# Kernel optimization log

Hardware: AMD Instinct MI355X
Metric: run time of the kernel (lower is better)

The kernel has to match this reference:

```python
import jax, jax.numpy as jnp
import numpy as np

B, IN, H = 4096, 1024, 1024


def setup_inputs() -> dict:
    key = jax.random.key(0)
    ks = jax.random.split(key, 20)
    s_in = 1.0 / np.sqrt(IN)
    s_h = 1.0 / np.sqrt(H)
    def lin(kw, kb, fan_in, scale):
        W = jax.random.uniform(kw, (H, fan_in), jnp.float32, -scale, scale)
        b = jax.random.uniform(kb, (H,), jnp.float32, -scale, scale)
        return W, b
    Wxf, bxf = lin(ks[0], ks[1], IN, s_in)
    Whf, bhf = lin(ks[2], ks[3], H, s_h)
    Wxi, bxi = lin(ks[4], ks[5], IN, s_in)
    Whi, bhi = lin(ks[6], ks[7], H, s_h)
    Wxo, bxo = lin(ks[8], ks[9], IN, s_in)
    Who, bho = lin(ks[10], ks[11], H, s_h)
    Wxc, bxc = lin(ks[12], ks[13], IN, s_in)
    Whc, bhc = lin(ks[14], ks[15], H, s_h)
    x = jax.random.normal(ks[16], (B, IN), jnp.float32)
    c = jax.random.normal(ks[17], (B, H), jnp.float32)
    h = jax.random.normal(ks[18], (B, H), jnp.float32)
    return dict(x=x, c=c, h=h,
                Wxf=Wxf, bxf=bxf, Whf=Whf, bhf=bhf,
                Wxi=Wxi, bxi=bxi, Whi=Whi, bhi=bhi,
                Wxo=Wxo, bxo=bxo, Who=Who, bho=bho,
                Wxc=Wxc, bxc=bxc, Whc=Whc, bhc=bhc)


def reference(x, c, h,
              Wxf, bxf, Whf, bhf,
              Wxi, bxi, Whi, bhi,
              Wxo, bxo, Who, bho,
              Wxc, bxc, Whc, bhc):
    # Fuse the 8 small GEMMs into two batched GEMMs: x @ Wx^T and h @ Wh^T
    # with gate outputs concatenated along the hidden dim [f, i, o, c~].
    Wx = jnp.concatenate([Wxf, Wxi, Wxo, Wxc], axis=0)   # [4H, IN]
    Wh = jnp.concatenate([Whf, Whi, Who, Whc], axis=0)   # [4H, H]
    bx = jnp.concatenate([bxf, bxi, bxo, bxc], axis=0)   # [4H]
    bh = jnp.concatenate([bhf, bhi, bho, bhc], axis=0)   # [4H]
    gates = x @ Wx.T + h @ Wh.T + (bx + bh)              # [B, 4H]
    hs = Wxf.shape[0]
    f = jax.nn.sigmoid(gates[:, 0 * hs:1 * hs])
    i = jax.nn.sigmoid(gates[:, 1 * hs:2 * hs])
    o = jax.nn.sigmoid(gates[:, 2 * hs:3 * hs])
    ctil = jnp.tanh(gates[:, 3 * hs:4 * hs])
    ct = f * c + ctil * i
    ht = jnp.tanh(ct) * o
    return (ct, ht)
```

## Files before the change

kernel.cpp:

```cpp
#include <hip/hip_runtime.h>
#include <hip/hip_bf16.h>
#include <stdint.h>

typedef __hip_bfloat16 bf16;
typedef __attribute__((ext_vector_type(8))) short short8;
typedef __attribute__((ext_vector_type(16))) float floatx16;

#define AS1(p) ((const __attribute__((address_space(1))) void*)(p))
#define AS3(p) ((__attribute__((address_space(3))) void*)(p))

#define M_DIM 4096
#define H_DIM 1024
#define STAGE 24576

__device__ __forceinline__ unsigned short f2bf(float f) {
    uint32_t u = __float_as_uint(f);
    uint32_t r = (u + 0x7FFFu + ((u >> 16) & 1u)) >> 16;
    return (unsigned short)r;
}
__device__ __forceinline__ float fast_sigmoid(float v) {
    return 1.0f / (1.0f + __expf(-v));
}
__device__ __forceinline__ float fast_tanh(float v) {
    return 2.0f / (1.0f + __expf(-2.0f * v)) - 1.0f;
}

__global__ __launch_bounds__(256)
void pack_bf16(const float* __restrict__ x, const float* __restrict__ h,
               const float* Wxf, const float* Wxi, const float* Wxo, const float* Wxc,
               const float* Whf, const float* Whi, const float* Who, const float* Whc,
               unsigned short* __restrict__ ws)
{
    const int w = threadIdx.x >> 6;
    const int l = threadIdx.x & 63;
    const uint32_t W = blockIdx.x * 4u + (uint32_t)w;

    const uint32_t r  = (uint32_t)l & 31u;
    const uint32_t kh = (uint32_t)l >> 5;

    const float* src;
    uint32_t row, kq;
    if (W < 16384u) {
        const uint32_t ch4 = W & 3u;
        kq = (W >> 2) & 127u;
        const uint32_t mx = W >> 9;
        src = (kq < 64u) ? x : h;
        row = mx * 128u + ch4 * 32u + r;
    } else {
        const uint32_t V  = W - 16384u;
        kq = V & 127u;
        const uint32_t U  = V >> 7;
        const uint32_t b8 = U & 7u;
        const uint32_t ny = U >> 3;
        const uint32_t g  = b8 >> 1;
        const uint32_t nh = b8 & 1u;
        if (kq < 64u)
            src = (g == 0) ? Wxf : (g == 1) ? Wxi : (g == 2) ? Wxo : Wxc;
        else
            src = (g == 0) ? Whf : (g == 1) ? Whi : (g == 2) ? Who : Whc;
        row = ny * 64u + nh * 32u + r;
    }
    const float* s = src + (size_t)row * 1024u + (kq & 63u) * 16u + kh * 8u;
    const float4 v0 = *(const float4*)s;
    const float4 v1 = *(const float4*)(s + 4);
    short8 pk;
    pk[0] = (short)f2bf(v0.x); pk[1] = (short)f2bf(v0.y);
    pk[2] = (short)f2bf(v0.z); pk[3] = (short)f2bf(v0.w);
    pk[4] = (short)f2bf(v1.x); pk[5] = (short)f2bf(v1.y);
    pk[6] = (short)f2bf(v1.z); pk[7] = (short)f2bf(v1.w);
    *(short8*)(ws + (size_t)W * 512u + (uint32_t)l * 8u) = pk;
}

#define GLL(srcp, dstp) __builtin_amdgcn_global_load_lds(AS1(srcp), AS3(dstp), 16, 0, 0)
#define WAITB(N) do {                                                         \
    asm volatile("s_waitcnt vmcnt(" #N ") lgkmcnt(0)\ns_barrier" ::: "memory");\
    __builtin_amdgcn_sched_barrier(0);                                        \
} while (0)

#define MFMA32(a, b, c) __builtin_amdgcn_mfma_f32_32x32x16_bf16((a), (b), (c), 0, 0, 0)

#define ISSUE(SL) do {                                                        \
    GLL(p0, lds + (SL)*STAGE + loff0); p0 += ks0;                             \
    GLL(p1, lds + (SL)*STAGE + loff1); p1 += ks1;                             \
    GLL(p2, lds + (SL)*STAGE + loff2); p2 += ks2;                             \
} while (0)

#define COMPUTE(SC) do {                                                      \
    short8 a0_ = *(const short8*)(ldsA + (SC)*STAGE + 0);                     \
    short8 a1_ = *(const short8*)(ldsA + (SC)*STAGE + 1024);                  \
    short8 b0_ = *(const short8*)(ldsB + (SC)*STAGE + 0);                     \
    short8 b1_ = *(const short8*)(ldsB + (SC)*STAGE + 2048);                  \
    acc00 = MFMA32(a0_, b0_, acc00);                                          \
    acc01 = MFMA32(a1_, b0_, acc01);                                          \
    acc10 = MFMA32(a0_, b1_, acc10);                                          \
    acc11 = MFMA32(a1_, b1_, acc11);                                          \
    a0_ = *(const short8*)(ldsA + (SC)*STAGE + 4096);                         \
    a1_ = *(const short8*)(ldsA + (SC)*STAGE + 4096 + 1024);                  \
    b0_ = *(const short8*)(ldsB + (SC)*STAGE + 8192);                         \
    b1_ = *(const short8*)(ldsB + (SC)*STAGE + 8192 + 2048);                  \
    acc00 = MFMA32(a0_, b0_, acc00);                                          \
    acc01 = MFMA32(a1_, b0_, acc01);                                          \
    acc10 = MFMA32(a0_, b1_, acc10);                                          \
    acc11 = MFMA32(a1_, b1_, acc11);                                          \
} while (0)

#define ITER(SC, SL) do { WAITB(3); ISSUE(SL); COMPUTE(SC); } while (0)

__global__ __launch_bounds__(512, 4)
void lstm_fused_kernel(const unsigned short* __restrict__ ws,
                       const float* __restrict__ c,
                       const float* __restrict__ bxf, const float* __restrict__ bhf,
                       const float* __restrict__ bxi, const float* __restrict__ bhi,
                       const float* __restrict__ bxo, const float* __restrict__ bho,
                       const float* __restrict__ bxc, const float* __restrict__ bhc,
                       float* __restrict__ out)
{
    __shared__ __align__(16) char lds[3 * STAGE];

    const int tid  = threadIdx.x;
    const int w    = tid >> 6;
    const int lane = tid & 63;

    const int bid = blockIdx.x;
    const int mx  = bid >> 4;
    const int ny  = ((bid & 7) << 1) | ((bid >> 3) & 1);
    const int bm0 = mx * 128;
    const int bn0 = ny * 64;

    const int wM = w >> 2;
    const int wN = (w >> 1) & 1;
    const int gp = w & 1;

    const unsigned short* p0; const unsigned short* p1; const unsigned short* p2;
    uint32_t loff0, loff1, loff2, ks0, ks1, ks2;
#define CHDEC(CH, P, LO, KS) do {                                             \
    const int ch_ = (CH);                                                     \
    if (ch_ < 8) {                                                            \
        const uint32_t kc_ = (uint32_t)ch_ >> 2, c4_ = (uint32_t)ch_ & 3u;    \
        P = ws + ((uint32_t)mx * 512u + kc_ * 4u + c4_) * 512u                \
               + (uint32_t)lane * 8u;                                         \
        KS = 4096u;                                                           \
    } else {                                                                  \
        const uint32_t b_ = (uint32_t)(ch_ - 8), kc_ = b_ >> 3, b8_ = b_ & 7u;\
        P = ws + (16384u + ((uint32_t)ny * 8u + b8_) * 128u + kc_) * 512u     \
               + (uint32_t)lane * 8u;                                         \
        KS = 1024u;                                                           \
    }                                                                         \
    LO = (uint32_t)ch_ * 1024u;                                               \
} while (0)
    CHDEC(w * 3 + 0, p0, loff0, ks0);
    CHDEC(w * 3 + 1, p1, loff1, ks1);
    CHDEC(w * 3 + 2, p2, loff2, ks2);
#undef CHDEC

    const char* ldsA = lds + (uint32_t)lane * 16u + (uint32_t)wM * 2048u;
    const char* ldsB = lds + (uint32_t)lane * 16u + 8192u
                           + ((uint32_t)(4 * gp + wN)) * 1024u;

    floatx16 acc00 = {0}, acc01 = {0}, acc10 = {0}, acc11 = {0};

    ISSUE(0);
    ISSUE(1);

    for (int t = 0; t < 20; ++t) {
        ITER(0, 2); ITER(1, 0); ITER(2, 1);
    }
    ITER(0, 2);
    ITER(1, 0);
    WAITB(3); COMPUTE(2);
    WAITB(0); COMPUTE(0);

    const int colg = bn0 + (wN * 32) + (lane & 31);
    const int lq   = lane >> 5;
    const int wrow = wM * 64;
    float* out_ct = out;
    float* out_ht = out + (size_t)M_DIM * H_DIM;

    float bA, bB;
    if (gp == 0) { bA = bxf[colg] + bhf[colg]; bB = bxi[colg] + bhi[colg]; }
    else         { bA = bxo[colg] + bho[colg]; bB = bxc[colg] + bhc[colg]; }

    if (gp == 0) {
#pragma unroll
        for (int r = 0; r < 16; ++r) {
            acc00[r] = fast_sigmoid(acc00[r] + bA);
            acc01[r] = fast_sigmoid(acc01[r] + bA);
            acc10[r] = fast_sigmoid(acc10[r] + bB);
            acc11[r] = fast_sigmoid(acc11[r] + bB);
        }
    } else {
#pragma unroll
        for (int r = 0; r < 16; ++r) {
            acc00[r] = fast_sigmoid(acc00[r] + bA);
            acc01[r] = fast_sigmoid(acc01[r] + bA);
            acc10[r] = fast_tanh(acc10[r] + bB);
            acc11[r] = fast_tanh(acc11[r] + bB);
        }
    }

    __syncthreads();

    {
        char* wr = (char*)lds + (uint32_t)(w >> 1) * 16384u + (uint32_t)gp * 8192u;
        if (gp == 0) {
#pragma unroll
            for (int r = 0; r < 16; ++r) {
                const int ri = (r & 3) + 8 * (r >> 2) + 4 * lq;
                *(float*)(wr +        ri * 128 + (lane & 31) * 4) = acc01[r];
                *(float*)(wr + 4096 + ri * 128 + (lane & 31) * 4) = acc11[r];
            }
        } else {
#pragma unroll
            for (int r = 0; r < 16; ++r) {
                const int ri = (r & 3) + 8 * (r >> 2) + 4 * lq;
                *(float*)(wr +        ri * 128 + (lane & 31) * 4) = acc00[r];
                *(float*)(wr + 4096 + ri * 128 + (lane & 31) * 4) = acc10[r];
            }
        }
    }

    __syncthreads();

    {
        const char* rd = (const char*)lds + (uint32_t)(w >> 1) * 16384u
                                          + (uint32_t)(1 - gp) * 8192u;
        if (gp == 0) {
#pragma unroll
            for (int r = 0; r < 16; ++r) {
                const int ri = (r & 3) + 8 * (r >> 2) + 4 * lq;
                const float O  = *(const float*)(rd +        ri * 128 + (lane & 31) * 4);
                const float CT = *(const float*)(rd + 4096 + ri * 128 + (lane & 31) * 4);
                const int row = bm0 + wrow + ri;
                const float cv  = c[(size_t)row * H_DIM + colg];
                const float ctn = acc00[r] * cv + CT * acc10[r];
                const float htn = fast_tanh(ctn) * O;
                out_ct[(size_t)row * H_DIM + colg] = ctn;
                out_ht[(size_t)row * H_DIM + colg] = htn;
            }
        } else {
#pragma unroll
            for (int r = 0; r < 16; ++r) {
                const int ri = (r & 3) + 8 * (r >> 2) + 4 * lq;
                const float F = *(const float*)(rd +        ri * 128 + (lane & 31) * 4);
                const float I = *(const float*)(rd + 4096 + ri * 128 + (lane & 31) * 4);
                const int row = bm0 + wrow + 32 + ri;
                const float cv  = c[(size_t)row * H_DIM + colg];
                const float ctn = F * cv + acc11[r] * I;
                const float htn = fast_tanh(ctn) * acc01[r];
                out_ct[(size_t)row * H_DIM + colg] = ctn;
                out_ht[(size_t)row * H_DIM + colg] = htn;
            }
        }
    }
}

extern "C" void kernel_launch(void* const* d_in, const int* in_sizes, int n_in,
                              void* d_out, int out_size, void* d_ws, size_t ws_size,
                              hipStream_t stream) {
    (void)in_sizes; (void)n_in; (void)out_size; (void)ws_size;
    const float* x   = (const float*)d_in[0];
    const float* c   = (const float*)d_in[1];
    const float* h   = (const float*)d_in[2];
    const float* Wxf = (const float*)d_in[3];  const float* bxf = (const float*)d_in[4];
    const float* Whf = (const float*)d_in[5];  const float* bhf = (const float*)d_in[6];
    const float* Wxi = (const float*)d_in[7];  const float* bxi = (const float*)d_in[8];
    const float* Whi = (const float*)d_in[9];  const float* bhi = (const float*)d_in[10];
    const float* Wxo = (const float*)d_in[11]; const float* bxo = (const float*)d_in[12];
    const float* Who = (const float*)d_in[13]; const float* bho = (const float*)d_in[14];
    const float* Wxc = (const float*)d_in[15]; const float* bxc = (const float*)d_in[16];
    const float* Whc = (const float*)d_in[17]; const float* bhc = (const float*)d_in[18];
    float* out = (float*)d_out;
    unsigned short* ws = (unsigned short*)d_ws;

    pack_bf16<<<8192, 256, 0, stream>>>(x, h,
        Wxf, Wxi, Wxo, Wxc, Whf, Whi, Who, Whc, ws);

    lstm_fused_kernel<<<512, 512, 0, stream>>>(ws, c,
        bxf, bhf, bxi, bhi, bxo, bho, bxc, bhc, out);
}
```

Baseline: 247.5 us.

## Assign all four gates per wave to remove LDS epilogue exchange

Changes the per-wave MFMA tiling so each wave computes a 32x32 tile for all four gates (one A fragment, four B fragments) instead of a 64x64 tile for two gates. With f, i, o and c~ all held in the same wave's registers, the epilogue no longer needs two __syncthreads and an LDS round-trip to exchange gate values between paired waves. The cost is more LDS reads of B per MFMA in the main loop (one A read per four B reads instead of two A and two B), which changes LDS bandwidth pressure.

New measurement: 228.3 us. 1.08x faster.

```diff
diff --git a/kernel.cpp b/kernel.cpp
--- a/kernel.cpp
+++ b/kernel.cpp
@@ -86,22 +86,24 @@
 } while (0)
 
 #define COMPUTE(SC) do {                                                      \
-    short8 a0_ = *(const short8*)(ldsA + (SC)*STAGE + 0);                     \
-    short8 a1_ = *(const short8*)(ldsA + (SC)*STAGE + 1024);                  \
+    short8 a_  = *(const short8*)(ldsA + (SC)*STAGE + 0);                     \
     short8 b0_ = *(const short8*)(ldsB + (SC)*STAGE + 0);                     \
     short8 b1_ = *(const short8*)(ldsB + (SC)*STAGE + 2048);                  \
-    acc00 = MFMA32(a0_, b0_, acc00);                                          \
-    acc01 = MFMA32(a1_, b0_, acc01);                                          \
-    acc10 = MFMA32(a0_, b1_, acc10);                                          \
-    acc11 = MFMA32(a1_, b1_, acc11);                                          \
-    a0_ = *(const short8*)(ldsA + (SC)*STAGE + 4096);                         \
-    a1_ = *(const short8*)(ldsA + (SC)*STAGE + 4096 + 1024);                  \
+    short8 b2_ = *(const short8*)(ldsB + (SC)*STAGE + 4096);                  \
+    short8 b3_ = *(const short8*)(ldsB + (SC)*STAGE + 6144);                  \
+    acc0 = MFMA32(a_, b0_, acc0);                                             \
+    acc1 = MFMA32(a_, b1_, acc1);                                             \
+    acc2 = MFMA32(a_, b2_, acc2);                                             \
+    acc3 = MFMA32(a_, b3_, acc3);                                             \
+    a_  = *(const short8*)(ldsA + (SC)*STAGE + 4096);                         \
     b0_ = *(const short8*)(ldsB + (SC)*STAGE + 8192);                         \
     b1_ = *(const short8*)(ldsB + (SC)*STAGE + 8192 + 2048);                  \
-    acc00 = MFMA32(a0_, b0_, acc00);                                          \
-    acc01 = MFMA32(a1_, b0_, acc01);                                          \
-    acc10 = MFMA32(a0_, b1_, acc10);                                          \
-    acc11 = MFMA32(a1_, b1_, acc11);                                          \
+    b2_ = *(const short8*)(ldsB + (SC)*STAGE + 8192 + 4096);                  \
+    b3_ = *(const short8*)(ldsB + (SC)*STAGE + 8192 + 6144);                  \
+    acc0 = MFMA32(a_, b0_, acc0);                                             \
+    acc1 = MFMA32(a_, b1_, acc1);                                             \
+    acc2 = MFMA32(a_, b2_, acc2);                                             \
+    acc3 = MFMA32(a_, b3_, acc3);                                             \
 } while (0)
 
 #define ITER(SC, SL) do { WAITB(3); ISSUE(SL); COMPUTE(SC); } while (0)
@@ -127,9 +129,8 @@
     const int bm0 = mx * 128;
     const int bn0 = ny * 64;
 
-    const int wM = w >> 2;
-    const int wN = (w >> 1) & 1;
-    const int gp = w & 1;
+    const int wM2 = w >> 1;
+    const int wN  = w & 1;
 
     const unsigned short* p0; const unsigned short* p1; const unsigned short* p2;
     uint32_t loff0, loff1, loff2, ks0, ks1, ks2;
@@ -153,11 +154,10 @@
     CHDEC(w * 3 + 2, p2, loff2, ks2);
 #undef CHDEC
 
-    const char* ldsA = lds + (uint32_t)lane * 16u + (uint32_t)wM * 2048u;
-    const char* ldsB = lds + (uint32_t)lane * 16u + 8192u
-                           + ((uint32_t)(4 * gp + wN)) * 1024u;
-
-    floatx16 acc00 = {0}, acc01 = {0}, acc10 = {0}, acc11 = {0};
+    const char* ldsA = lds + (uint32_t)lane * 16u + (uint32_t)wM2 * 1024u;
+    const char* ldsB = lds + (uint32_t)lane * 16u + 8192u + (uint32_t)wN * 1024u;
+
+    floatx16 acc0 = {0}, acc1 = {0}, acc2 = {0}, acc3 = {0};
 
     ISSUE(0);
     ISSUE(1);
@@ -170,87 +170,30 @@
     WAITB(3); COMPUTE(2);
     WAITB(0); COMPUTE(0);
 
-    const int colg = bn0 + (wN * 32) + (lane & 31);
+    const int colg = bn0 + wN * 32 + (lane & 31);
     const int lq   = lane >> 5;
-    const int wrow = wM * 64;
+    const int row0 = bm0 + wM2 * 32;
     float* out_ct = out;
     float* out_ht = out + (size_t)M_DIM * H_DIM;
 
-    float bA, bB;
-    if (gp == 0) { bA = bxf[colg] + bhf[colg]; bB = bxi[colg] + bhi[colg]; }
-    else         { bA = bxo[colg] + bho[colg]; bB = bxc[colg] + bhc[colg]; }
-
-    if (gp == 0) {
+    const float bf_ = bxf[colg] + bhf[colg];
+    const float bi_ = bxi[colg] + bhi[colg];
+    const float bo_ = bxo[colg] + bho[colg];
+    const float bc_ = bxc[colg] + bhc[colg];
+
 #pragma unroll
-        for (int r = 0; r < 16; ++r) {
-            acc00[r] = fast_sigmoid(acc00[r] + bA);
-            acc01[r] = fast_sigmoid(acc01[r] + bA);
-            acc10[r] = fast_sigmoid(acc10[r] + bB);
-            acc11[r] = fast_sigmoid(acc11[r] + bB);
-        }
-    } else {
-#pragma unroll
-        for (int r = 0; r < 16; ++r) {
-            acc00[r] = fast_sigmoid(acc00[r] + bA);
-            acc01[r] = fast_sigmoid(acc01[r] + bA);
-            acc10[r] = fast_tanh(acc10[r] + bB);
-            acc11[r] = fast_tanh(acc11[r] + bB);
-        }
-    }
-
-    __syncthreads();
-
-    {
-        char* wr = (char*)lds + (uint32_t)(w >> 1) * 16384u + (uint32_t)gp * 8192u;
-        if (gp == 0) {
-#pragma unroll
-            for (int r = 0; r < 16; ++r) {
-                const int ri = (r & 3) + 8 * (r >> 2) + 4 * lq;
-                *(float*)(wr +        ri * 128 + (lane & 31) * 4) = acc01[r];
-                *(float*)(wr + 4096 + ri * 128 + (lane & 31) * 4) = acc11[r];
-            }
-        } else {
-#pragma unroll
-            for (int r = 0; r < 16; ++r) {
-                const int ri = (r & 3) + 8 * (r >> 2) + 4 * lq;
-                *(float*)(wr +        ri * 128 + (lane & 31) * 4) = acc00[r];
-                *(float*)(wr + 4096 + ri * 128 + (lane & 31) * 4) = acc10[r];
-            }
-        }
-    }
-
-    __syncthreads();
-
-    {
-        const char* rd = (const char*)lds + (uint32_t)(w >> 1) * 16384u
-                                          + (uint32_t)(1 - gp) * 8192u;
-        if (gp == 0) {
-#pragma unroll
-            for (int r = 0; r < 16; ++r) {
-                const int ri = (r & 3) + 8 * (r >> 2) + 4 * lq;
-                const float O  = *(const float*)(rd +        ri * 128 + (lane & 31) * 4);
-                const float CT = *(const float*)(rd + 4096 + ri * 128 + (lane & 31) * 4);
-                const int row = bm0 + wrow + ri;
-                const float cv  = c[(size_t)row * H_DIM + colg];
-                const float ctn = acc00[r] * cv + CT * acc10[r];
-                const float htn = fast_tanh(ctn) * O;
-                out_ct[(size_t)row * H_DIM + colg] = ctn;
-                out_ht[(size_t)row * H_DIM + colg] = htn;
-            }
-        } else {
-#pragma unroll
-            for (int r = 0; r < 16; ++r) {
-                const int ri = (r & 3) + 8 * (r >> 2) + 4 * lq;
-                const float F = *(const float*)(rd +        ri * 128 + (lane & 31) * 4);
-                const float I = *(const float*)(rd + 4096 + ri * 128 + (lane & 31) * 4);
-                const int row = bm0 + wrow + 32 + ri;
-                const float cv  = c[(size_t)row * H_DIM + colg];
-                const float ctn = F * cv + acc11[r] * I;
-                const float htn = fast_tanh(ctn) * acc01[r];
-                out_ct[(size_t)row * H_DIM + colg] = ctn;
-                out_ht[(size_t)row * H_DIM + colg] = htn;
-            }
-        }
+    for (int r = 0; r < 16; ++r) {
+        const int ri  = (r & 3) + 8 * (r >> 2) + 4 * lq;
+        const int row = row0 + ri;
+        const float f    = fast_sigmoid(acc0[r] + bf_);
+        const float ii   = fast_sigmoid(acc1[r] + bi_);
+        const float o    = fast_sigmoid(acc2[r] + bo_);
+        const float ctil = fast_tanh(acc3[r] + bc_);
+        const float cv   = c[(size_t)row * H_DIM + colg];
+        const float ctn  = f * cv + ctil * ii;
+        const float htn  = fast_tanh(ctn) * o;
+        out_ct[(size_t)row * H_DIM + colg] = ctn;
+        out_ht[(size_t)row * H_DIM + colg] = htn;
     }
 }
 
```
